# Performance work log

Measured on AMD Instinct MI355X. Metric: run time of the kernel, lower is better.

The kernel has to match this reference:

```python
import jax, jax.numpy as jnp
import numpy as np


def setup_inputs() -> dict:
    key = jax.random.key(0)
    k = jax.random.split(key, 5)
    B, D, T = 8, 512, 8192
    Dh = D // 8
    return {
        "x": jax.random.normal(k[0], (B, D, T), dtype=jnp.float32),
        "w1": jax.random.normal(k[1], (Dh, D), dtype=jnp.float32) * (1.0 / np.sqrt(D)),
        "b1": jax.random.normal(k[2], (Dh,), dtype=jnp.float32) * 0.01,
        "w2": jax.random.normal(k[3], (D, Dh), dtype=jnp.float32) * (1.0 / np.sqrt(Dh)),
        "b2": jax.random.normal(k[4], (D,), dtype=jnp.float32) * 0.01,
        "chunksize": 16,
    }


def reference(x, w1, b1, w2, b2, chunksize):
    # x: [B, D, T]
    B, D, T = x.shape
    pad = (T + chunksize - 1) // chunksize * chunksize - T  # static under jit
    Tp = T + pad
    xp = jnp.pad(x, ((0, 0), (0, 0), (0, pad)))
    # causal cumulative average over time
    denom = jnp.arange(1, Tp + 1, dtype=x.dtype)
    avg = jnp.cumsum(xp, axis=2) / denom  # [B, D, Tp]
    pooled = avg[:, :, chunksize - 1::chunksize]  # [B, D, Tc]
    # SE bottleneck (1x1 convs)
    h = jax.nn.relu(jnp.einsum('od,bdt->bot', w1, pooled) + b1[:, None])
    g = jax.nn.sigmoid(jnp.einsum('od,bdt->bot', w2, h) + b2[:, None])  # [B, D, Tc]
    # upsample gate to per-frame resolution and apply to residual
    up = jnp.repeat(g, chunksize, axis=2)[:, :, :T]
    return up * x
```

## Files before the change

kernel.cpp:

```cpp
#include <hip/hip_runtime.h>
#include <math.h>

#define BB 8
#define DD 512
#define DH 64
#define TT 8192
#define CS 16
#define CC 512

typedef float vf4 __attribute__((ext_vector_type(4)));

__device__ __forceinline__ float sigf(float v) {
    return 1.0f / (1.0f + __expf(-v));
}

__global__ __launch_bounds__(256) void k_pool_tr(
        const float* __restrict__ x, float* __restrict__ pooled,
        const float* __restrict__ w1, const float* __restrict__ w2,
        float* __restrict__ w1t, float* __restrict__ w2t) {
    const int blk = blockIdx.x;
    const int t = threadIdx.x;

    if (blk >= 4096) {
        int i = (blk - 4096) * 256 + t;
        int o = i & 63, d = i >> 6;
        w1t[i] = w1[o * DD + d];
        int o2 = i & 511, oo = i >> 9;
        w2t[i] = w2[o2 * DH + oo];
        return;
    }

    const int row = blk;
    const float4* xr = (const float4*)(x + (size_t)row * TT);

    __shared__ float psum[2048];
    __shared__ float wtot[4];

    #pragma unroll
    for (int k = 0; k < 8; k++) {
        float4 v = xr[t + k * 256];
        psum[t + k * 256] = (v.x + v.y) + (v.z + v.w);
    }
    __syncthreads();

    const float4* ps4 = (const float4*)psum;
    float4 q0 = ps4[2 * t];
    float4 q1 = ps4[2 * t + 1];
    float c0 = (q0.x + q0.y) + (q0.z + q0.w);
    float c1 = (q1.x + q1.y) + (q1.z + q1.w);

    float ps = c0 + c1;
    float v = ps;
    int lane = t & 63;
    #pragma unroll
    for (int off = 1; off < 64; off <<= 1) {
        float n = __shfl_up(v, off, 64);
        if (lane >= off) v += n;
    }
    int wid = t >> 6;
    if (lane == 63) wtot[wid] = v;
    __syncthreads();
    float wpre = 0.0f;
    for (int w = 0; w < wid; w++) wpre += wtot[w];
    float incl = v + wpre;
    float excl = incl - ps;
    float s0 = excl + c0;
    float s1 = s0 + c1;
    int c = 2 * t;
    float2 outv;
    outv.x = s0 / (float)(CS * (c + 1));
    outv.y = s1 / (float)(CS * (c + 2));
    ((float2*)(pooled + (size_t)row * CC))[t] = outv;
}

#define PSTR 516

__global__ __launch_bounds__(256) void k_segemm(
        const float* __restrict__ pooled,
        const float* __restrict__ w1t, const float* __restrict__ b1,
        const float* __restrict__ w2t, const float* __restrict__ b2,
        float* __restrict__ g) {
    const int b = blockIdx.y;
    const int c0 = blockIdx.x * 4;
    const int t = threadIdx.x;

    __shared__ float p[4 * PSTR];
    __shared__ float hs[DH * 4];

    {
        const float4* src = (const float4*)(pooled + (size_t)b * DD * CC + c0);
        float4 v0 = src[(size_t)t * (CC / 4)];
        float4 v1 = src[((size_t)t + 256) * (CC / 4)];
        p[0 * PSTR + t] = v0.x; p[1 * PSTR + t] = v0.y;
        p[2 * PSTR + t] = v0.z; p[3 * PSTR + t] = v0.w;
        p[0 * PSTR + t + 256] = v1.x; p[1 * PSTR + t + 256] = v1.y;
        p[2 * PSTR + t + 256] = v1.z; p[3 * PSTR + t + 256] = v1.w;
    }
    __syncthreads();

    const int o = t >> 2, c = t & 3;
    const float4* pc = (const float4*)(p + c * PSTR);
    float a0 = 0.f, a1 = 0.f, a2 = 0.f, a3 = 0.f;
    #pragma unroll 4
    for (int d4 = 0; d4 < 128; d4++) {
        float4 pv = pc[d4];
        int d = d4 * 4;
        a0 = fmaf(w1t[(d + 0) * DH + o], pv.x, a0);
        a1 = fmaf(w1t[(d + 1) * DH + o], pv.y, a1);
        a2 = fmaf(w1t[(d + 2) * DH + o], pv.z, a2);
        a3 = fmaf(w1t[(d + 3) * DH + o], pv.w, a3);
    }
    float hv = ((a0 + a1) + (a2 + a3)) + b1[o];
    hs[t] = fmaxf(hv, 0.0f);
    __syncthreads();

    float g00 = 0, g01 = 0, g02 = 0, g03 = 0;
    float g10 = 0, g11 = 0, g12 = 0, g13 = 0;
    const float4* h4 = (const float4*)hs;
    #pragma unroll 8
    for (int oo = 0; oo < DH; oo++) {
        float wv0 = w2t[oo * DD + t];
        float wv1 = w2t[oo * DD + t + 256];
        float4 h = h4[oo];
        g00 = fmaf(wv0, h.x, g00); g01 = fmaf(wv0, h.y, g01);
        g02 = fmaf(wv0, h.z, g02); g03 = fmaf(wv0, h.w, g03);
        g10 = fmaf(wv1, h.x, g10); g11 = fmaf(wv1, h.y, g11);
        g12 = fmaf(wv1, h.z, g12); g13 = fmaf(wv1, h.w, g13);
    }
    float bb0 = b2[t], bb1 = b2[t + 256];
    float4 r0, r1;
    r0.x = sigf(g00 + bb0); r0.y = sigf(g01 + bb0);
    r0.z = sigf(g02 + bb0); r0.w = sigf(g03 + bb0);
    r1.x = sigf(g10 + bb1); r1.y = sigf(g11 + bb1);
    r1.z = sigf(g12 + bb1); r1.w = sigf(g13 + bb1);
    float4* gp = (float4*)(g + (size_t)b * DD * CC + c0);
    gp[(size_t)t * (CC / 4)] = r0;
    gp[((size_t)t + 256) * (CC / 4)] = r1;
}

__global__ __launch_bounds__(256) void k_gate(
        const float* __restrict__ x, const float* __restrict__ g,
        float* __restrict__ out) {
    size_t i8 = (size_t)blockIdx.x * 256 + threadIdx.x;
    size_t i4 = i8 * 2;
    const vf4* x4 = (const vf4*)x;
    vf4 a = x4[i4];
    vf4 b = x4[i4 + 1];
    size_t row = i8 >> 10;
    int c = (int)((i8 & 1023) >> 1);
    float gv = g[row * CC + c];
    a *= gv;
    b *= gv;
    vf4* o4 = (vf4*)out;
    __builtin_nontemporal_store(a, o4 + i4);
    __builtin_nontemporal_store(b, o4 + i4 + 1);
}

extern "C" void kernel_launch(void* const* d_in, const int* in_sizes, int n_in,
                              void* d_out, int out_size, void* d_ws, size_t ws_size,
                              hipStream_t stream) {
    const float* x  = (const float*)d_in[0];
    const float* w1 = (const float*)d_in[1];
    const float* b1 = (const float*)d_in[2];
    const float* w2 = (const float*)d_in[3];
    const float* b2 = (const float*)d_in[4];
    float* out = (float*)d_out;

    char* ws = (char*)d_ws;
    float* pooled = (float*)(ws);
    float* g      = (float*)(ws + (size_t)BB * DD * CC * 4);
    float* w1t    = (float*)(ws + (size_t)2 * BB * DD * CC * 4);
    float* w2t    = (float*)(ws + (size_t)2 * BB * DD * CC * 4 + DH * DD * 4);

    k_pool_tr<<<dim3(4096 + 128), dim3(256), 0, stream>>>(x, pooled, w1, w2, w1t, w2t);
    k_segemm<<<dim3(CC / 4, BB), dim3(256), 0, stream>>>(pooled, w1t, b1, w2t, b2, g);
    k_gate<<<dim3(BB * DD * TT / 8 / 256), dim3(256), 0, stream>>>(x, g, out);
}
```

Measured before the change: 307.0 us.

## Fuse pool, SE GEMM and gate into one persistent kernel with grid barriers

Merges the three launches into a single persistent kernel of 512 blocks that synchronise through atomic grid barriers in workspace memory, reset by a memset before each launch. Each block pools eight rows, then computes two SE chunk tiles, then runs a grid-stride gate loop. The aim is to remove launch gaps and inter-kernel drains. In exchange, occupancy is capped by the persistent grid, the barriers spin-wait, and the gate stores no longer use nontemporal hints. Correctness depends on all 512 blocks being co-resident at once.

```diff
diff --git a/kernel.cpp b/kernel.cpp
--- a/kernel.cpp
+++ b/kernel.cpp
@@ -7,6 +7,8 @@
 #define TT 8192
 #define CS 16
 #define CC 512
+#define NBLK 512
+#define NTHR 256
 
 typedef float vf4 __attribute__((ext_vector_type(4)));
 
@@ -14,146 +16,156 @@
     return 1.0f / (1.0f + __expf(-v));
 }
 
-__global__ __launch_bounds__(256) void k_pool_tr(
-        const float* __restrict__ x, float* __restrict__ pooled,
-        const float* __restrict__ w1, const float* __restrict__ w2,
-        float* __restrict__ w1t, float* __restrict__ w2t) {
+__device__ __forceinline__ void grid_barrier(unsigned* cnt, unsigned nblocks) {
+    __syncthreads();
+    if (threadIdx.x == 0) {
+        __threadfence();
+        __hip_atomic_fetch_add(cnt, 1u, __ATOMIC_ACQ_REL, __HIP_MEMORY_SCOPE_AGENT);
+        while (__hip_atomic_load(cnt, __ATOMIC_ACQUIRE, __HIP_MEMORY_SCOPE_AGENT) < nblocks) {}
+    }
+    __syncthreads();
+}
+
+#define PSTR 516
+
+__global__ __launch_bounds__(256, 2) void k_fused(
+        const float* __restrict__ x,
+        const float* __restrict__ w1, const float* __restrict__ b1,
+        const float* __restrict__ w2, const float* __restrict__ b2,
+        float* __restrict__ out,
+        float* __restrict__ pooled, float* __restrict__ g,
+        float* __restrict__ w1t, float* __restrict__ w2t,
+        unsigned* __restrict__ bar) {
     const int blk = blockIdx.x;
     const int t = threadIdx.x;
 
-    if (blk >= 4096) {
-        int i = (blk - 4096) * 256 + t;
+    __shared__ float psum[2048];
+    __shared__ float wtot[4];
+    __shared__ float p[4 * PSTR];
+    __shared__ float hs[DH * 4];
+
+    if (blk < 128) {
+        int i = blk * 256 + t;
         int o = i & 63, d = i >> 6;
         w1t[i] = w1[o * DD + d];
         int o2 = i & 511, oo = i >> 9;
         w2t[i] = w2[o2 * DH + oo];
-        return;
+    }
+    for (int r = 0; r < 8; ++r) {
+        const int row = blk * 8 + r;
+        const float4* xr = (const float4*)(x + (size_t)row * TT);
+        #pragma unroll
+        for (int k = 0; k < 8; k++) {
+            float4 v = xr[t + k * 256];
+            psum[t + k * 256] = (v.x + v.y) + (v.z + v.w);
+        }
+        __syncthreads();
+        const float4* ps4 = (const float4*)psum;
+        float4 q0 = ps4[2 * t];
+        float4 q1 = ps4[2 * t + 1];
+        float c0 = (q0.x + q0.y) + (q0.z + q0.w);
+        float c1 = (q1.x + q1.y) + (q1.z + q1.w);
+        float ps = c0 + c1;
+        float v = ps;
+        int lane = t & 63;
+        #pragma unroll
+        for (int off = 1; off < 64; off <<= 1) {
+            float n = __shfl_up(v, off, 64);
+            if (lane >= off) v += n;
+        }
+        int wid = t >> 6;
+        if (lane == 63) wtot[wid] = v;
+        __syncthreads();
+        float wpre = 0.0f;
+        for (int w = 0; w < wid; w++) wpre += wtot[w];
+        float incl = v + wpre;
+        float excl = incl - ps;
+        float s0 = excl + c0;
+        float s1 = s0 + c1;
+        int c = 2 * t;
+        float2 outv;
+        outv.x = s0 / (float)(CS * (c + 1));
+        outv.y = s1 / (float)(CS * (c + 2));
+        ((float2*)(pooled + (size_t)row * CC))[t] = outv;
     }
 
-    const int row = blk;
-    const float4* xr = (const float4*)(x + (size_t)row * TT);
+    grid_barrier(bar + 0, NBLK);
 
-    __shared__ float psum[2048];
-    __shared__ float wtot[4];
+    for (int u = blk * 2; u < blk * 2 + 2; ++u) {
+        const int b = u >> 7;
+        const int c0i = (u & 127) * 4;
+        __syncthreads();
+        {
+            const float4* src = (const float4*)(pooled + (size_t)b * DD * CC + c0i);
+            float4 v0 = src[(size_t)t * (CC / 4)];
+            float4 v1 = src[((size_t)t + 256) * (CC / 4)];
+            p[0 * PSTR + t] = v0.x; p[1 * PSTR + t] = v0.y;
+            p[2 * PSTR + t] = v0.z; p[3 * PSTR + t] = v0.w;
+            p[0 * PSTR + t + 256] = v1.x; p[1 * PSTR + t + 256] = v1.y;
+            p[2 * PSTR + t + 256] = v1.z; p[3 * PSTR + t + 256] = v1.w;
+        }
+        __syncthreads();
 
-    #pragma unroll
-    for (int k = 0; k < 8; k++) {
-        float4 v = xr[t + k * 256];
-        psum[t + k * 256] = (v.x + v.y) + (v.z + v.w);
+        const int o = t >> 2, c = t & 3;
+        const float4* pc = (const float4*)(p + c * PSTR);
+        float a0 = 0.f, a1 = 0.f, a2 = 0.f, a3 = 0.f;
+        #pragma unroll 4
+        for (int d4 = 0; d4 < 128; d4++) {
+            float4 pv = pc[d4];
+            int d = d4 * 4;
+            a0 = fmaf(w1t[(d + 0) * DH + o], pv.x, a0);
+            a1 = fmaf(w1t[(d + 1) * DH + o], pv.y, a1);
+            a2 = fmaf(w1t[(d + 2) * DH + o], pv.z, a2);
+            a3 = fmaf(w1t[(d + 3) * DH + o], pv.w, a3);
+        }
+        float hv = ((a0 + a1) + (a2 + a3)) + b1[o];
+        hs[t] = fmaxf(hv, 0.0f);
+        __syncthreads();
+
+        float g00 = 0, g01 = 0, g02 = 0, g03 = 0;
+        float g10 = 0, g11 = 0, g12 = 0, g13 = 0;
+        const float4* h4 = (const float4*)hs;
+        #pragma unroll 8
+        for (int oo = 0; oo < DH; oo++) {
+            float wv0 = w2t[oo * DD + t];
+            float wv1 = w2t[oo * DD + t + 256];
+            float4 h = h4[oo];
+            g00 = fmaf(wv0, h.x, g00); g01 = fmaf(wv0, h.y, g01);
+            g02 = fmaf(wv0, h.z, g02); g03 = fmaf(wv0, h.w, g03);
+            g10 = fmaf(wv1, h.x, g10); g11 = fmaf(wv1, h.y, g11);
+            g12 = fmaf(wv1, h.z, g12); g13 = fmaf(wv1, h.w, g13);
+        }
+        float bb0 = b2[t], bb1 = b2[t + 256];
+        float4 r0, r1;
+        r0.x = sigf(g00 + bb0); r0.y = sigf(g01 + bb0);
+        r0.z = sigf(g02 + bb0); r0.w = sigf(g03 + bb0);
+        r1.x = sigf(g10 + bb1); r1.y = sigf(g11 + bb1);
+        r1.z = sigf(g12 + bb1); r1.w = sigf(g13 + bb1);
+        float4* gp = (float4*)(g + (size_t)b * DD * CC + c0i);
+        gp[(size_t)t * (CC / 4)] = r0;
+        gp[((size_t)t + 256) * (CC / 4)] = r1;
     }
-    __syncthreads();
 
-    const float4* ps4 = (const float4*)psum;
-    float4 q0 = ps4[2 * t];
-    float4 q1 = ps4[2 * t + 1];
-    float c0 = (q0.x + q0.y) + (q0.z + q0.w);
-    float c1 = (q1.x + q1.y) + (q1.z + q1.w);
-
-    float ps = c0 + c1;
-    float v = ps;
-    int lane = t & 63;
-    #pragma unroll
-    for (int off = 1; off < 64; off <<= 1) {
-        float n = __shfl_up(v, off, 64);
-        if (lane >= off) v += n;
-    }
-    int wid = t >> 6;
-    if (lane == 63) wtot[wid] = v;
-    __syncthreads();
-    float wpre = 0.0f;
-    for (int w = 0; w < wid; w++) wpre += wtot[w];
-    float incl = v + wpre;
-    float excl = incl - ps;
-    float s0 = excl + c0;
-    float s1 = s0 + c1;
-    int c = 2 * t;
-    float2 outv;
-    outv.x = s0 / (float)(CS * (c + 1));
-    outv.y = s1 / (float)(CS * (c + 2));
-    ((float2*)(pooled + (size_t)row * CC))[t] = outv;
-}
-
-#define PSTR 516
-
-__global__ __launch_bounds__(256) void k_segemm(
-        const float* __restrict__ pooled,
-        const float* __restrict__ w1t, const float* __restrict__ b1,
-        const float* __restrict__ w2t, const float* __restrict__ b2,
-        float* __restrict__ g) {
-    const int b = blockIdx.y;
-    const int c0 = blockIdx.x * 4;
-    const int t = threadIdx.x;
-
-    __shared__ float p[4 * PSTR];
-    __shared__ float hs[DH * 4];
+    grid_barrier(bar + 1, NBLK);
 
     {
-        const float4* src = (const float4*)(pooled + (size_t)b * DD * CC + c0);
-        float4 v0 = src[(size_t)t * (CC / 4)];
-        float4 v1 = src[((size_t)t + 256) * (CC / 4)];
-        p[0 * PSTR + t] = v0.x; p[1 * PSTR + t] = v0.y;
-        p[2 * PSTR + t] = v0.z; p[3 * PSTR + t] = v0.w;
-        p[0 * PSTR + t + 256] = v1.x; p[1 * PSTR + t + 256] = v1.y;
-        p[2 * PSTR + t + 256] = v1.z; p[3 * PSTR + t + 256] = v1.w;
+        const size_t total8 = (size_t)BB * DD * TT / 8;
+        const vf4* x4 = (const vf4*)x;
+        vf4* o4 = (vf4*)out;
+        for (size_t i8 = (size_t)blk * NTHR + t; i8 < total8;
+             i8 += (size_t)NBLK * NTHR) {
+            size_t i4 = i8 * 2;
+            vf4 a = x4[i4];
+            vf4 bv = x4[i4 + 1];
+            size_t row = i8 >> 10;
+            int c = (int)((i8 & 1023) >> 1);
+            float gv = g[row * CC + c];
+            a *= gv;
+            bv *= gv;
+            o4[i4] = a;
+            o4[i4 + 1] = bv;
+        }
     }
-    __syncthreads();
-
-    const int o = t >> 2, c = t & 3;
-    const float4* pc = (const float4*)(p + c * PSTR);
-    float a0 = 0.f, a1 = 0.f, a2 = 0.f, a3 = 0.f;
-    #pragma unroll 4
-    for (int d4 = 0; d4 < 128; d4++) {
-        float4 pv = pc[d4];
-        int d = d4 * 4;
-        a0 = fmaf(w1t[(d + 0) * DH + o], pv.x, a0);
-        a1 = fmaf(w1t[(d + 1) * DH + o], pv.y, a1);
-        a2 = fmaf(w1t[(d + 2) * DH + o], pv.z, a2);
-        a3 = fmaf(w1t[(d + 3) * DH + o], pv.w, a3);
-    }
-    float hv = ((a0 + a1) + (a2 + a3)) + b1[o];
-    hs[t] = fmaxf(hv, 0.0f);
-    __syncthreads();
-
-    float g00 = 0, g01 = 0, g02 = 0, g03 = 0;
-    float g10 = 0, g11 = 0, g12 = 0, g13 = 0;
-    const float4* h4 = (const float4*)hs;
-    #pragma unroll 8
-    for (int oo = 0; oo < DH; oo++) {
-        float wv0 = w2t[oo * DD + t];
-        float wv1 = w2t[oo * DD + t + 256];
-        float4 h = h4[oo];
-        g00 = fmaf(wv0, h.x, g00); g01 = fmaf(wv0, h.y, g01);
-        g02 = fmaf(wv0, h.z, g02); g03 = fmaf(wv0, h.w, g03);
-        g10 = fmaf(wv1, h.x, g10); g11 = fmaf(wv1, h.y, g11);
-        g12 = fmaf(wv1, h.z, g12); g13 = fmaf(wv1, h.w, g13);
-    }
-    float bb0 = b2[t], bb1 = b2[t + 256];
-    float4 r0, r1;
-    r0.x = sigf(g00 + bb0); r0.y = sigf(g01 + bb0);
-    r0.z = sigf(g02 + bb0); r0.w = sigf(g03 + bb0);
-    r1.x = sigf(g10 + bb1); r1.y = sigf(g11 + bb1);
-    r1.z = sigf(g12 + bb1); r1.w = sigf(g13 + bb1);
-    float4* gp = (float4*)(g + (size_t)b * DD * CC + c0);
-    gp[(size_t)t * (CC / 4)] = r0;
-    gp[((size_t)t + 256) * (CC / 4)] = r1;
-}
-
-__global__ __launch_bounds__(256) void k_gate(
-        const float* __restrict__ x, const float* __restrict__ g,
-        float* __restrict__ out) {
-    size_t i8 = (size_t)blockIdx.x * 256 + threadIdx.x;
-    size_t i4 = i8 * 2;
-    const vf4* x4 = (const vf4*)x;
-    vf4 a = x4[i4];
-    vf4 b = x4[i4 + 1];
-    size_t row = i8 >> 10;
-    int c = (int)((i8 & 1023) >> 1);
-    float gv = g[row * CC + c];
-    a *= gv;
-    b *= gv;
-    vf4* o4 = (vf4*)out;
-    __builtin_nontemporal_store(a, o4 + i4);
-    __builtin_nontemporal_store(b, o4 + i4 + 1);
 }
 
 extern "C" void kernel_launch(void* const* d_in, const int* in_sizes, int n_in,
@@ -171,8 +183,9 @@
     float* g      = (float*)(ws + (size_t)BB * DD * CC * 4);
     float* w1t    = (float*)(ws + (size_t)2 * BB * DD * CC * 4);
     float* w2t    = (float*)(ws + (size_t)2 * BB * DD * CC * 4 + DH * DD * 4);
+    unsigned* bar = (unsigned*)(ws + (size_t)2 * BB * DD * CC * 4 + 2 * DH * DD * 4);
 
-    k_pool_tr<<<dim3(4096 + 128), dim3(256), 0, stream>>>(x, pooled, w1, w2, w1t, w2t);
-    k_segemm<<<dim3(CC / 4, BB), dim3(256), 0, stream>>>(pooled, w1t, b1, w2t, b2, g);
-    k_gate<<<dim3(BB * DD * TT / 8 / 256), dim3(256), 0, stream>>>(x, g, out);
+    hipMemsetAsync(bar, 0, 64, stream);
+    k_fused<<<dim3(NBLK), dim3(NTHR), 0, stream>>>(
+        x, w1, b1, w2, b2, out, pooled, g, w1t, w2t, bar);
 }
```

Measured after the change: 448.0 us. +45.9%, slower.
